# Kernel optimization log

Measured on AMD Instinct MI355X. Metric: run time of the kernel, lower is better.

The kernel has to match this reference:

```python
import jax, jax.numpy as jnp
import numpy as np
import math

D_MODEL = 1024
NUM_HEADS = 16
D_K = D_MODEL // NUM_HEADS


def setup_inputs() -> dict:
    key = jax.random.key(0)
    ks = jax.random.split(key, 7)
    B, S = 2, 2048
    scale = 1.0 / math.sqrt(D_MODEL)
    inp = {
        "q": jax.random.normal(ks[0], (B, S, D_MODEL), dtype=jnp.float32),
        "k": jax.random.normal(ks[1], (B, S, D_MODEL), dtype=jnp.float32),
        "v": jax.random.normal(ks[2], (B, S, D_MODEL), dtype=jnp.float32),
        # Source module reuses q_linear for q, k, and v projections, so only
        # Wq/bq are needed for the input projections; out projection separate.
        "Wq": jax.random.normal(ks[3], (D_MODEL, D_MODEL), dtype=jnp.float32) * scale,
        "bq": jnp.zeros((D_MODEL,), dtype=jnp.float32),
        "Wo": jax.random.normal(ks[4], (D_MODEL, D_MODEL), dtype=jnp.float32) * scale,
        "bo": jnp.zeros((D_MODEL,), dtype=jnp.float32),
    }
    return inp


def _attention(q, k, v, Wq, bq, Wo, bo):
    B, S, _ = q.shape

    def proj(x):
        # [B,S,D] -> [B,H,S,d_k]
        y = jnp.einsum("bsd,de->bse", x, Wq) + bq
        return y.reshape(B, S, NUM_HEADS, D_K).transpose(0, 2, 1, 3)

    qh, kh, vh = proj(q), proj(k), proj(v)
    # scores: [B,H,S,S]
    scores = jnp.einsum("bhsd,bhtd->bhst", qh, kh) / math.sqrt(D_K)
    attn = jax.nn.softmax(scores, axis=-1)
    # dropout: eval-mode identity
    out = jnp.einsum("bhst,bhtd->bhsd", attn, vh)  # [B,H,S,d_k]
    out = out.transpose(0, 2, 1, 3).reshape(B, S, D_MODEL)
    return jnp.einsum("bsd,de->bse", out, Wo) + bo


def reference(q, k, v, Wq, bq, Wo, bo):
    return _attention(q, k, v, Wq, bq, Wo, bo)
```

## Files before the change

kernel.cpp:

```cpp
#include <hip/hip_runtime.h>
#include <hip/hip_bf16.h>

typedef unsigned short u16;
typedef unsigned int   u32;
typedef __attribute__((ext_vector_type(8))) short bf16x8;
typedef __attribute__((ext_vector_type(4))) float f32x4;
typedef __attribute__((ext_vector_type(16))) float f32x16;

#define SEQ     2048
#define DM      1024
#define NH      16
#define DKH     64
#define PER_SRC 4194304

#define OFF_VT   0u
#define OFF_AOH  8388608u
#define OFF_WQT  25165824u
#define OFF_WOT  27262976u
#define OFF_QH   29360128u
#define OFF_KH   37748736u
#define OFF_VH   46137344u
#define OFF_PML  46137344u
#define OFF_PO   54525952u
#define NEED_WS  88080384u
#define PART_O_U 4194304
#define PART_ML_F 131072

__device__ __forceinline__ u16 f2bf(float f) {
    union { float f; u32 u; } c; c.f = f;
    return (u16)((c.u + 0x7fffu + ((c.u >> 16) & 1u)) >> 16);
}

__device__ __forceinline__ float bf2f(u16 h) {
    union { u32 u; float f; } c; c.u = (u32)h << 16;
    return c.f;
}

__device__ __forceinline__ u32 cvt_pk_bf16(float lo, float hi) {
    u32 r;
    asm("v_cvt_pk_bf16_f32 %0, %1, %2" : "=v"(r) : "v"(lo), "v"(hi));
    return r;
}

__device__ __forceinline__ void gload_lds16(const void* g, void* l) {
    __builtin_amdgcn_global_load_lds((__attribute__((address_space(1))) void*)g,
                                     (__attribute__((address_space(3))) void*)l,
                                     16, 0, 0);
}

__global__ void cast_qkv(const float* __restrict__ q, const float* __restrict__ k,
                         const float* __restrict__ v, u16* __restrict__ xb) {
    const float* src = (blockIdx.y == 0) ? q : (blockIdx.y == 1) ? k : v;
    u16* dst = xb + (size_t)blockIdx.y * PER_SRC;
    size_t i = ((size_t)blockIdx.x * 256 + threadIdx.x) * 8;
    float4 a = *(const float4*)(src + i);
    float4 b = *(const float4*)(src + i + 4);
    bf16x8 o;
    o[0] = (short)f2bf(a.x); o[1] = (short)f2bf(a.y);
    o[2] = (short)f2bf(a.z); o[3] = (short)f2bf(a.w);
    o[4] = (short)f2bf(b.x); o[5] = (short)f2bf(b.y);
    o[6] = (short)f2bf(b.z); o[7] = (short)f2bf(b.w);
    *(bf16x8*)(dst + i) = o;
}

__global__ void wtrans(const float* __restrict__ Wq, const float* __restrict__ Wo,
                       u16* __restrict__ Wqt, u16* __restrict__ Wot) {
    const float* W = blockIdx.y ? Wo : Wq;
    u16* Wt       = blockIdx.y ? Wot : Wqt;
    int k0 = (blockIdx.x & 15) * 64;
    int n0 = (blockIdx.x >> 4) * 64;
    __shared__ __align__(16) float t[64][68];
    int tid = threadIdx.x;
    int r = tid >> 2, cs = (tid & 3) * 16;
    #pragma unroll
    for (int j = 0; j < 4; ++j) {
        float4 vv = *(const float4*)(W + (size_t)(k0 + r) * DM + n0 + cs + j * 4);
        *(float4*)&t[r][cs + j * 4] = vv;
    }
    __syncthreads();
    bf16x8 o0, o1;
    #pragma unroll
    for (int j = 0; j < 8; ++j) o0[j] = (short)f2bf(t[cs + j][r]);
    #pragma unroll
    for (int j = 0; j < 8; ++j) o1[j] = (short)f2bf(t[cs + 8 + j][r]);
    u16* dst = Wt + (size_t)(n0 + r) * DM + k0 + cs;
    *(bf16x8*)(dst)     = o0;
    *(bf16x8*)(dst + 8) = o1;
}

__global__ void vtrans(const u16* __restrict__ vh, u16* __restrict__ vt) {
    int bh = blockIdx.y, st = blockIdx.x;
    __shared__ u16 t[64][72];
    int tid = threadIdx.x;
    int r = tid >> 2, cs = (tid & 3) * 16;
    const u16* src = vh + ((size_t)bh * SEQ + st * 64 + r) * DKH + cs;
    bf16x8 v0 = *(const bf16x8*)(src);
    bf16x8 v1 = *(const bf16x8*)(src + 8);
    #pragma unroll
    for (int j = 0; j < 8; ++j) { t[r][cs + j] = (u16)v0[j]; t[r][cs + 8 + j] = (u16)v1[j]; }
    __syncthreads();
    bf16x8 o0, o1;
    #pragma unroll
    for (int j = 0; j < 8; ++j) o0[j] = (short)t[cs + j][r];
    #pragma unroll
    for (int j = 0; j < 8; ++j) o1[j] = (short)t[cs + 8 + j][r];
    bf16x8 w0, w1;
    #pragma unroll
    for (int j = 0; j < 4; ++j) {
        w0[j] = o0[j];     w0[4 + j] = o1[j];
        w1[j] = o0[4 + j]; w1[4 + j] = o1[4 + j];
    }
    u16* dst = vt + ((size_t)bh * DKH + r) * SEQ + st * 64 + cs;
    *(bf16x8*)(dst)     = w0;
    *(bf16x8*)(dst + 8) = w1;
}

template<int MODE>
__global__ __launch_bounds__(256)
void gemm_bt(const u16* __restrict__ Abase, const u16* __restrict__ Bt,
             const float* __restrict__ bias, void* __restrict__ outbase)
{
    __shared__ __align__(16) u16 Alds[128 * 64];
    __shared__ __align__(16) u16 Blds[128 * 64];

    const int tid  = threadIdx.x;
    const int wave = tid >> 6;
    const int lane = tid & 63;
    const int low4 = lane & 15;
    const int quad = lane >> 4;
    const int bid  = blockIdx.x;
    const int xcd  = bid & 7;
    const int j    = bid >> 3;
    const int m0 = (xcd * 4 + (j >> 3)) * 128;
    const int n0 = (j & 7) * 128;
    const int wm = (wave >> 1) * 64, wn = (wave & 1) * 64;

    const u16* A = Abase + (size_t)blockIdx.z * PER_SRC;

    f32x4 acc[4][4] = {};

    for (int kt = 0; kt < DM / 64; ++kt) {
        #pragma unroll
        for (int it = 0; it < 4; ++it) {
            int seg  = it * 256 + tid;
            int row  = seg >> 3;
            int slot = seg & 7;
            int ss   = slot ^ (row & 7);
            const u16* srcA;
            if (MODE == 0) {
                srcA = A + (size_t)(m0 + row) * DM + kt * 64 + ss * 8;
            } else {
                int m = m0 + row;
                srcA = A + (((size_t)((m >> 11) * NH + kt)) * SEQ + (m & (SEQ - 1))) * DKH + ss * 8;
            }
            gload_lds16(srcA, &Alds[(it * 256 + wave * 64) * 8]);
            gload_lds16(Bt + (size_t)(n0 + row) * DM + kt * 64 + ss * 8,
                        &Blds[(it * 256 + wave * 64) * 8]);
        }
        __syncthreads();
        #pragma unroll
        for (int kk = 0; kk < 2; ++kk) {
            bf16x8 af[4], bfr[4];
            #pragma unroll
            for (int mi = 0; mi < 4; ++mi) {
                int row = wm + mi * 16 + low4;
                af[mi] = *(const bf16x8*)&Alds[row * 64 + (((kk * 4 + quad) ^ (row & 7)) * 8)];
            }
            #pragma unroll
            for (int ni = 0; ni < 4; ++ni) {
                int row = wn + ni * 16 + low4;
                bfr[ni] = *(const bf16x8*)&Blds[row * 64 + (((kk * 4 + quad) ^ (row & 7)) * 8)];
            }
            #pragma unroll
            for (int mi = 0; mi < 4; ++mi)
                #pragma unroll
                for (int ni = 0; ni < 4; ++ni)
                    acc[mi][ni] = __builtin_amdgcn_mfma_f32_16x16x32_bf16(
                        af[mi], bfr[ni], acc[mi][ni], 0, 0, 0);
        }
        __syncthreads();
    }

    #pragma unroll
    for (int mi = 0; mi < 4; ++mi) {
        #pragma unroll
        for (int ni = 0; ni < 4; ++ni) {
            int n = n0 + wn + ni * 16 + low4;
            float bv = bias[n];
            #pragma unroll
            for (int j2 = 0; j2 < 4; ++j2) {
                int m = m0 + wm + mi * 16 + quad * 4 + j2;
                float val = acc[mi][ni][j2] + bv;
                if (MODE == 0) {
                    u16* dst = (u16*)outbase + (size_t)blockIdx.z * PER_SRC;
                    int b = m >> 11, s = m & (SEQ - 1);
                    int h = n >> 6, dd = n & 63;
                    dst[(size_t)(b * NH + h) * (SEQ * DKH) + (size_t)s * DKH + dd] = f2bf(val);
                } else {
                    ((float*)outbase)[(size_t)m * DM + n] = val;
                }
            }
        }
    }
}

template<int SPLIT>
__global__ __launch_bounds__(256, 2)
void attn(const u16* __restrict__ qh, const u16* __restrict__ kh,
          const u16* __restrict__ vt, u16* __restrict__ aoh,
          u16* __restrict__ pOb, float* __restrict__ pml)
{
    __shared__ __align__(16) u16 lds[2][8192];

    const int tid  = threadIdx.x;
    const int w    = tid >> 6;
    const int lane = tid & 63;
    const int l31  = lane & 31;
    const int hi   = lane >> 5;

    int bid = blockIdx.x;
    int lid = (bid & 7) * 64 + (bid >> 3);
    const int qt = lid & 15;
    const int bh = lid >> 4;
    const int part = SPLIT ? blockIdx.y : 0;
    const int kt0  = SPLIT ? part * 8 : 0;
    const int nkt  = SPLIT ? 8 : 32;

    const int qbase = qt * 128 + w * 32;
    const int q_row = qbase + l31;

    const float SC = 0.18033688f;

    bf16x8 qf[4];
    #pragma unroll
    for (int c = 0; c < 4; ++c)
        qf[c] = *(const bf16x8*)&qh[((size_t)bh * SEQ + q_row) * DKH + c * 16 + hi * 8];

    float m_r = -1e30f, l_r = 0.f;
    f32x16 ot[2] = {};

#define STAGE(buf, kt_)                                                                 \
    {                                                                                   \
        _Pragma("unroll")                                                               \
        for (int it = 0; it < 2; ++it) {                                                \
            int seg  = it * 256 + tid;                                                  \
            int row  = seg >> 3;                                                        \
            int slot = seg & 7;                                                         \
            int ss   = slot ^ (row & 7);                                                \
            gload_lds16(kh + ((size_t)bh * SEQ + (kt_) * 64 + row) * DKH + ss * 8,      \
                        &lds[buf][(it * 256 + w * 64) * 8]);                            \
            gload_lds16(vt + ((size_t)bh * DKH + row) * SEQ + (kt_) * 64 + ss * 8,      \
                        &lds[buf][4096 + (it * 256 + w * 64) * 8]);                     \
        }                                                                               \
    }

    STAGE(0, kt0);
    __syncthreads();

    int cur = 0;
    for (int ki = 0; ki < nkt; ++ki) {
        if (ki + 1 < nkt) STAGE(cur ^ 1, kt0 + ki + 1);

        const u16* Klds = &lds[cur][0];
        const u16* Vlds = &lds[cur][4096];

        f32x16 st[2];
        #pragma unroll
        for (int T = 0; T < 2; ++T) {
            f32x16 acc = {};
            __builtin_amdgcn_s_setprio(1);
            #pragma unroll
            for (int c = 0; c < 4; ++c) {
                int row = T * 32 + l31;
                bf16x8 kf = *(const bf16x8*)&Klds[row * 64 + (((c * 2 + hi) ^ (row & 7)) * 8)];
                acc = __builtin_amdgcn_mfma_f32_32x32x16_bf16(kf, qf[c], acc, 0, 0, 0);
            }
            __builtin_amdgcn_s_setprio(0);
            st[T] = acc;
        }

        float mx[8];
        #pragma unroll
        for (int r = 0; r < 8; ++r)
            mx[r] = fmaxf(fmaxf(st[0][r], st[0][r + 8]),
                          fmaxf(st[1][r], st[1][r + 8]));
        float t0 = fmaxf(fmaxf(mx[0], mx[1]), mx[2]);
        float t1 = fmaxf(fmaxf(mx[3], mx[4]), mx[5]);
        float t2 = fmaxf(mx[6], mx[7]);
        float lmax = fmaxf(fmaxf(t0, t1), t2);
        float mloc = fmaxf(lmax, __shfl_xor(lmax, 32)) * SC;

        float mnew = fmaxf(m_r, mloc);
        if (!__all(mloc <= m_r + 11.5f)) {
            float fac = __builtin_amdgcn_exp2f(m_r - mnew);
            m_r = mnew;
            l_r *= fac;
            #pragma unroll
            for (int dt = 0; dt < 2; ++dt)
                #pragma unroll
                for (int r = 0; r < 16; ++r) ot[dt][r] *= fac;
        }

        float nm = -m_r;
        float rs0 = 0.f, rs1 = 0.f, rs2 = 0.f, rs3 = 0.f;
        #pragma unroll
        for (int T = 0; T < 2; ++T)
            #pragma unroll
            for (int r = 0; r < 16; r += 4) {
                float p0 = __builtin_amdgcn_exp2f(fmaf(st[T][r],     SC, nm));
                float p1 = __builtin_amdgcn_exp2f(fmaf(st[T][r + 1], SC, nm));
                float p2 = __builtin_amdgcn_exp2f(fmaf(st[T][r + 2], SC, nm));
                float p3 = __builtin_amdgcn_exp2f(fmaf(st[T][r + 3], SC, nm));
                st[T][r] = p0; st[T][r + 1] = p1; st[T][r + 2] = p2; st[T][r + 3] = p3;
                rs0 += p0; rs1 += p1; rs2 += p2; rs3 += p3;
            }
        float rsum = (rs0 + rs1) + (rs2 + rs3);
        l_r += rsum + __shfl_xor(rsum, 32);

        u32 pk[2][8];
        #pragma unroll
        for (int T = 0; T < 2; ++T)
            #pragma unroll
            for (int g = 0; g < 8; ++g)
                pk[T][g] = cvt_pk_bf16(st[T][2 * g], st[T][2 * g + 1]);

        __builtin_amdgcn_s_setprio(1);
        #pragma unroll
        for (int dt = 0; dt < 2; ++dt)
            #pragma unroll
            for (int c = 0; c < 4; ++c) {
                int row = dt * 32 + l31;
                bf16x8 vf = *(const bf16x8*)&Vlds[row * 64 + (((c * 2 + hi) ^ (row & 7)) * 8)];
                union { bf16x8 v; u32 u[4]; } pf;
                int T = c >> 1, g0 = (c & 1) * 4;
                pf.u[0] = pk[T][g0];     pf.u[1] = pk[T][g0 + 1];
                pf.u[2] = pk[T][g0 + 2]; pf.u[3] = pk[T][g0 + 3];
                ot[dt] = __builtin_amdgcn_mfma_f32_32x32x16_bf16(vf, pf.v, ot[dt], 0, 0, 0);
            }
        __builtin_amdgcn_s_setprio(0);

        __syncthreads();
        cur ^= 1;
    }

    float inv = (SPLIT == 0) ? (1.0f / l_r) : 1.0f;
    u16* dstb = (SPLIT == 0) ? aoh : (pOb + (size_t)part * PART_O_U);
    u16* tile = &lds[0][0] + w * 2048;
    #pragma unroll
    for (int dt = 0; dt < 2; ++dt)
        #pragma unroll
        for (int g = 0; g < 4; ++g) {
            u32 w0 = cvt_pk_bf16(ot[dt][4 * g] * inv,     ot[dt][4 * g + 1] * inv);
            u32 w1 = cvt_pk_bf16(ot[dt][4 * g + 2] * inv, ot[dt][4 * g + 3] * inv);
            int d0 = 8 * g + 4 * hi + 32 * dt;
            int byteoff = l31 * 128 + ((d0 * 2) ^ ((l31 & 7) << 4));
            uint2 pr; pr.x = w0; pr.y = w1;
            *(uint2*)((char*)tile + byteoff) = pr;
        }
    const size_t gbase = ((size_t)bh * SEQ + qbase) * DKH;
    #pragma unroll
    for (int p = 0; p < 4; ++p) {
        int q = p * 8 + (lane >> 3);
        int byteoff = q * 128 + (((lane & 7) * 16) ^ ((q & 7) << 4));
        bf16x8 val = *(const bf16x8*)((const char*)tile + byteoff);
        *(bf16x8*)&dstb[gbase + p * 512 + lane * 8] = val;
    }
    if (SPLIT == 1 && hi == 0) {
        float2 ml; ml.x = m_r; ml.y = l_r;
        *(float2*)&pml[(size_t)part * PART_ML_F + ((size_t)bh * SEQ + qbase + l31) * 2] = ml;
    }
#undef STAGE
}

__global__ __launch_bounds__(256)
void attn_merge(const u16* __restrict__ pOb, const float* __restrict__ pml,
                u16* __restrict__ aoh)
{
    int tid = threadIdx.x;
    int bh = blockIdx.x >> 5;
    int qb = blockIdx.x & 31;
    int ql = tid >> 2;
    int dc = tid & 3;
    size_t row = (size_t)bh * SEQ + qb * 64 + ql;

    float2 ml[4];
    #pragma unroll
    for (int p = 0; p < 4; ++p)
        ml[p] = *(const float2*)&pml[(size_t)p * PART_ML_F + row * 2];
    float m = fmaxf(fmaxf(ml[0].x, ml[1].x), fmaxf(ml[2].x, ml[3].x));
    float wgt[4];
    float denom = 0.f;
    #pragma unroll
    for (int p = 0; p < 4; ++p) {
        wgt[p] = __builtin_amdgcn_exp2f(ml[p].x - m);
        denom += wgt[p] * ml[p].y;
    }
    float invd = 1.0f / denom;
    #pragma unroll
    for (int p = 0; p < 4; ++p) wgt[p] *= invd;

    float acc[16];
    #pragma unroll
    for (int i = 0; i < 16; ++i) acc[i] = 0.f;
    #pragma unroll
    for (int p = 0; p < 4; ++p) {
        const u16* src = pOb + (size_t)p * PART_O_U + row * DKH + dc * 16;
        bf16x8 x0 = *(const bf16x8*)(src);
        bf16x8 x1 = *(const bf16x8*)(src + 8);
        #pragma unroll
        for (int i = 0; i < 8; ++i) {
            acc[i]     = fmaf(bf2f((u16)x0[i]), wgt[p], acc[i]);
            acc[8 + i] = fmaf(bf2f((u16)x1[i]), wgt[p], acc[8 + i]);
        }
    }
    u16* dst = aoh + row * DKH + dc * 16;
    u16 outv[16];
    #pragma unroll
    for (int i = 0; i < 16; ++i) outv[i] = f2bf(acc[i]);
    *(bf16x8*)(dst)     = *(bf16x8*)&outv[0];
    *(bf16x8*)(dst + 8) = *(bf16x8*)&outv[8];
}

extern "C" void kernel_launch(void* const* d_in, const int* in_sizes, int n_in,
                              void* d_out, int out_size, void* d_ws, size_t ws_size,
                              hipStream_t stream)
{
    const float* q  = (const float*)d_in[0];
    const float* k  = (const float*)d_in[1];
    const float* v  = (const float*)d_in[2];
    const float* Wq = (const float*)d_in[3];
    const float* bq = (const float*)d_in[4];
    const float* Wo = (const float*)d_in[5];
    const float* bo = (const float*)d_in[6];

    char* ws = (char*)d_ws;
    u16* xb  = (u16*)(ws);
    u16* wqt = (u16*)(ws + OFF_WQT);
    u16* wot = (u16*)(ws + OFF_WOT);
    u16* qh  = (u16*)(ws + OFF_QH);
    u16* kh  = (u16*)(ws + OFF_KH);
    u16* vh  = (u16*)(ws + OFF_VH);
    u16* vt  = (u16*)(ws + OFF_VT);
    u16* aoh = (u16*)(ws + OFF_AOH);
    u16* pOb = (u16*)(ws + OFF_PO);
    float* pml = (float*)(ws + OFF_PML);

    cast_qkv<<<dim3(2048, 3), dim3(256), 0, stream>>>(q, k, v, xb);
    wtrans<<<dim3(256, 2), dim3(256), 0, stream>>>(Wq, Wo, wqt, wot);
    gemm_bt<0><<<dim3(256, 1, 3), dim3(256), 0, stream>>>(xb, wqt, bq, (void*)qh);
    vtrans<<<dim3(32, 32), dim3(256), 0, stream>>>(vh, vt);
    if (ws_size >= (size_t)NEED_WS) {
        attn<1><<<dim3(512, 4), dim3(256), 0, stream>>>(qh, kh, vt, aoh, pOb, pml);
        attn_merge<<<dim3(1024), dim3(256), 0, stream>>>(pOb, pml, aoh);
    } else {
        attn<0><<<dim3(512), dim3(256), 0, stream>>>(qh, kh, vt, aoh, pOb, pml);
    }
    gemm_bt<1><<<dim3(256), dim3(256), 0, stream>>>(aoh, wot, bo, d_out);
}
```

Baseline: 141.6 us.

## Halve attention KV split and use smaller output-projection tiles for more blocks

The KV split-attention is reduced from four partitions to two. Each attention block now processes 16 KV tiles, and the merge kernel reads and rescales only two partial results, which cuts partial-output traffic and workspace needs. The output projection gets its own kernel with 64x128 tiles, launching 512 blocks instead of 256 so more of the GPU is occupied on that small GEMM. The trade-off is fewer attention blocks (1024) and less operand reuse per block in the output GEMM.

Result: faster. 132.7 us (-6.3%).

```diff
diff --git a/kernel.cpp b/kernel.cpp
--- a/kernel.cpp
+++ b/kernel.cpp
@@ -22,7 +22,7 @@
 #define OFF_VH   46137344u
 #define OFF_PML  46137344u
 #define OFF_PO   54525952u
-#define NEED_WS  88080384u
+#define NEED_WS  71303168u
 #define PART_O_U 4194304
 #define PART_ML_F 131072
 
@@ -115,10 +115,9 @@
     *(bf16x8*)(dst + 8) = w1;
 }
 
-template<int MODE>
 __global__ __launch_bounds__(256)
-void gemm_bt(const u16* __restrict__ Abase, const u16* __restrict__ Bt,
-             const float* __restrict__ bias, void* __restrict__ outbase)
+void gemm_qkv(const u16* __restrict__ Abase, const u16* __restrict__ Bt,
+              const float* __restrict__ bias, u16* __restrict__ outbase)
 {
     __shared__ __align__(16) u16 Alds[128 * 64];
     __shared__ __align__(16) u16 Blds[128 * 64];
@@ -146,14 +145,8 @@
             int row  = seg >> 3;
             int slot = seg & 7;
             int ss   = slot ^ (row & 7);
-            const u16* srcA;
-            if (MODE == 0) {
-                srcA = A + (size_t)(m0 + row) * DM + kt * 64 + ss * 8;
-            } else {
-                int m = m0 + row;
-                srcA = A + (((size_t)((m >> 11) * NH + kt)) * SEQ + (m & (SEQ - 1))) * DKH + ss * 8;
-            }
-            gload_lds16(srcA, &Alds[(it * 256 + wave * 64) * 8]);
+            gload_lds16(A + (size_t)(m0 + row) * DM + kt * 64 + ss * 8,
+                        &Alds[(it * 256 + wave * 64) * 8]);
             gload_lds16(Bt + (size_t)(n0 + row) * DM + kt * 64 + ss * 8,
                         &Blds[(it * 256 + wave * 64) * 8]);
         }
@@ -191,14 +184,91 @@
             for (int j2 = 0; j2 < 4; ++j2) {
                 int m = m0 + wm + mi * 16 + quad * 4 + j2;
                 float val = acc[mi][ni][j2] + bv;
-                if (MODE == 0) {
-                    u16* dst = (u16*)outbase + (size_t)blockIdx.z * PER_SRC;
-                    int b = m >> 11, s = m & (SEQ - 1);
-                    int h = n >> 6, dd = n & 63;
-                    dst[(size_t)(b * NH + h) * (SEQ * DKH) + (size_t)s * DKH + dd] = f2bf(val);
-                } else {
-                    ((float*)outbase)[(size_t)m * DM + n] = val;
-                }
+                u16* dst = outbase + (size_t)blockIdx.z * PER_SRC;
+                int b = m >> 11, s = m & (SEQ - 1);
+                int h = n >> 6, dd = n & 63;
+                dst[(size_t)(b * NH + h) * (SEQ * DKH) + (size_t)s * DKH + dd] = f2bf(val);
+            }
+        }
+    }
+}
+
+__global__ __launch_bounds__(256)
+void gemm_o(const u16* __restrict__ Abf, const u16* __restrict__ Bt,
+            const float* __restrict__ bias, float* __restrict__ out)
+{
+    __shared__ __align__(16) u16 Alds[64 * 64];
+    __shared__ __align__(16) u16 Blds[128 * 64];
+
+    const int tid  = threadIdx.x;
+    const int wave = tid >> 6;
+    const int lane = tid & 63;
+    const int low4 = lane & 15;
+    const int quad = lane >> 4;
+    const int bid  = blockIdx.x;
+    const int xcd  = bid & 7;
+    const int j    = bid >> 3;
+    const int m0 = (xcd * 8 + (j >> 3)) * 64;
+    const int n0 = (j & 7) * 128;
+    const int wm = (wave >> 1) * 32, wn = (wave & 1) * 64;
+
+    f32x4 acc[2][4] = {};
+
+    for (int kt = 0; kt < DM / 64; ++kt) {
+        #pragma unroll
+        for (int it = 0; it < 2; ++it) {
+            int seg  = it * 256 + tid;
+            int row  = seg >> 3;
+            int slot = seg & 7;
+            int ss   = slot ^ (row & 7);
+            int m = m0 + row;
+            const u16* srcA = Abf +
+                (((size_t)((m >> 11) * NH + kt)) * SEQ + (m & (SEQ - 1))) * DKH + ss * 8;
+            gload_lds16(srcA, &Alds[seg * 8]);
+        }
+        #pragma unroll
+        for (int it = 0; it < 4; ++it) {
+            int seg  = it * 256 + tid;
+            int row  = seg >> 3;
+            int slot = seg & 7;
+            int ss   = slot ^ (row & 7);
+            gload_lds16(Bt + (size_t)(n0 + row) * DM + kt * 64 + ss * 8,
+                        &Blds[seg * 8]);
+        }
+        __syncthreads();
+        #pragma unroll
+        for (int kk = 0; kk < 2; ++kk) {
+            bf16x8 af[2], bfr[4];
+            #pragma unroll
+            for (int mi = 0; mi < 2; ++mi) {
+                int row = wm + mi * 16 + low4;
+                af[mi] = *(const bf16x8*)&Alds[row * 64 + (((kk * 4 + quad) ^ (row & 7)) * 8)];
+            }
+            #pragma unroll
+            for (int ni = 0; ni < 4; ++ni) {
+                int row = wn + ni * 16 + low4;
+                bfr[ni] = *(const bf16x8*)&Blds[row * 64 + (((kk * 4 + quad) ^ (row & 7)) * 8)];
+            }
+            #pragma unroll
+            for (int mi = 0; mi < 2; ++mi)
+                #pragma unroll
+                for (int ni = 0; ni < 4; ++ni)
+                    acc[mi][ni] = __builtin_amdgcn_mfma_f32_16x16x32_bf16(
+                        af[mi], bfr[ni], acc[mi][ni], 0, 0, 0);
+        }
+        __syncthreads();
+    }
+
+    #pragma unroll
+    for (int mi = 0; mi < 2; ++mi) {
+        #pragma unroll
+        for (int ni = 0; ni < 4; ++ni) {
+            int n = n0 + wn + ni * 16 + low4;
+            float bv = bias[n];
+            #pragma unroll
+            for (int j2 = 0; j2 < 4; ++j2) {
+                int m = m0 + wm + mi * 16 + quad * 4 + j2;
+                out[(size_t)m * DM + n] = acc[mi][ni][j2] + bv;
             }
         }
     }
@@ -223,8 +293,8 @@
     const int qt = lid & 15;
     const int bh = lid >> 4;
     const int part = SPLIT ? blockIdx.y : 0;
-    const int kt0  = SPLIT ? part * 8 : 0;
-    const int nkt  = SPLIT ? 8 : 32;
+    const int kt0  = SPLIT ? part * 16 : 0;
+    const int nkt  = SPLIT ? 16 : 32;
 
     const int qbase = qt * 128 + w * 32;
     const int q_row = qbase + l31;
@@ -383,40 +453,25 @@
     int dc = tid & 3;
     size_t row = (size_t)bh * SEQ + qb * 64 + ql;
 
-    float2 ml[4];
-    #pragma unroll
-    for (int p = 0; p < 4; ++p)
-        ml[p] = *(const float2*)&pml[(size_t)p * PART_ML_F + row * 2];
-    float m = fmaxf(fmaxf(ml[0].x, ml[1].x), fmaxf(ml[2].x, ml[3].x));
-    float wgt[4];
-    float denom = 0.f;
-    #pragma unroll
-    for (int p = 0; p < 4; ++p) {
-        wgt[p] = __builtin_amdgcn_exp2f(ml[p].x - m);
-        denom += wgt[p] * ml[p].y;
-    }
-    float invd = 1.0f / denom;
-    #pragma unroll
-    for (int p = 0; p < 4; ++p) wgt[p] *= invd;
-
-    float acc[16];
-    #pragma unroll
-    for (int i = 0; i < 16; ++i) acc[i] = 0.f;
-    #pragma unroll
-    for (int p = 0; p < 4; ++p) {
-        const u16* src = pOb + (size_t)p * PART_O_U + row * DKH + dc * 16;
-        bf16x8 x0 = *(const bf16x8*)(src);
-        bf16x8 x1 = *(const bf16x8*)(src + 8);
-        #pragma unroll
-        for (int i = 0; i < 8; ++i) {
-            acc[i]     = fmaf(bf2f((u16)x0[i]), wgt[p], acc[i]);
-            acc[8 + i] = fmaf(bf2f((u16)x1[i]), wgt[p], acc[8 + i]);
-        }
+    float2 ml1 = *(const float2*)&pml[row * 2];
+    float2 ml2 = *(const float2*)&pml[PART_ML_F + row * 2];
+    float m  = fmaxf(ml1.x, ml2.x);
+    float w1 = __builtin_amdgcn_exp2f(ml1.x - m);
+    float w2 = __builtin_amdgcn_exp2f(ml2.x - m);
+    float inv = 1.0f / (ml1.y * w1 + ml2.y * w2);
+    float a1 = w1 * inv, a2 = w2 * inv;
+
+    const u16* s1 = pOb + row * DKH + dc * 16;
+    const u16* s2 = pOb + PART_O_U + row * DKH + dc * 16;
+    bf16x8 x0 = *(const bf16x8*)(s1), x1 = *(const bf16x8*)(s1 + 8);
+    bf16x8 y0 = *(const bf16x8*)(s2), y1 = *(const bf16x8*)(s2 + 8);
+    u16 outv[16];
+    #pragma unroll
+    for (int i = 0; i < 8; ++i) {
+        outv[i]     = f2bf(bf2f((u16)x0[i]) * a1 + bf2f((u16)y0[i]) * a2);
+        outv[8 + i] = f2bf(bf2f((u16)x1[i]) * a1 + bf2f((u16)y1[i]) * a2);
     }
     u16* dst = aoh + row * DKH + dc * 16;
-    u16 outv[16];
-    #pragma unroll
-    for (int i = 0; i < 16; ++i) outv[i] = f2bf(acc[i]);
     *(bf16x8*)(dst)     = *(bf16x8*)&outv[0];
     *(bf16x8*)(dst + 8) = *(bf16x8*)&outv[8];
 }
@@ -447,13 +502,13 @@
 
     cast_qkv<<<dim3(2048, 3), dim3(256), 0, stream>>>(q, k, v, xb);
     wtrans<<<dim3(256, 2), dim3(256), 0, stream>>>(Wq, Wo, wqt, wot);
-    gemm_bt<0><<<dim3(256, 1, 3), dim3(256), 0, stream>>>(xb, wqt, bq, (void*)qh);
+    gemm_qkv<<<dim3(256, 1, 3), dim3(256), 0, stream>>>(xb, wqt, bq, qh);
     vtrans<<<dim3(32, 32), dim3(256), 0, stream>>>(vh, vt);
     if (ws_size >= (size_t)NEED_WS) {
-        attn<1><<<dim3(512, 4), dim3(256), 0, stream>>>(qh, kh, vt, aoh, pOb, pml);
+        attn<1><<<dim3(512, 2), dim3(256), 0, stream>>>(qh, kh, vt, aoh, pOb, pml);
         attn_merge<<<dim3(1024), dim3(256), 0, stream>>>(pOb, pml, aoh);
     } else {
         attn<0><<<dim3(512), dim3(256), 0, stream>>>(qh, kh, vt, aoh, pOb, pml);
     }
-    gemm_bt<1><<<dim3(256), dim3(256), 0, stream>>>(aoh, wot, bo, d_out);
-}
+    gemm_o<<<dim3(512), dim3(256), 0, stream>>>(aoh, wot, bo, (float*)d_out);
+}
```
